# Kernel optimization log

Measured on AMD Instinct MI355X. Metric: run time of the kernel, lower is better.

Reference implementation:

```python
import jax, jax.numpy as jnp
import numpy as np

NUM_SRC = 200000
NUM_DST = 100000
NUM_EDGES = 1600000
IN_DIM = 128
HID = 256
OUT_DIM = 128


def layer_norm(h, g, b, eps=1e-5):
    mu = jnp.mean(h, axis=-1, keepdims=True)
    var = jnp.mean((h - mu) ** 2, axis=-1, keepdims=True)
    return (h - mu) * jax.lax.rsqrt(var + eps) * g + b


def setup_inputs() -> dict:
    key = jax.random.key(0)
    ks = jax.random.split(key, 8)
    s_in = 1.0 / np.sqrt(IN_DIM)
    s_hid = 1.0 / np.sqrt(HID)
    return {
        "x": jax.random.normal(ks[0], (NUM_SRC, IN_DIM), dtype=jnp.float32),
        "w_l": jax.random.normal(ks[1], (IN_DIM, HID), dtype=jnp.float32) * s_in,
        "b_l": jnp.zeros((HID,), dtype=jnp.float32),
        "w_r": jax.random.normal(ks[2], (IN_DIM, HID), dtype=jnp.float32) * s_in,
        "ln1_g": jnp.ones((HID,), dtype=jnp.float32),
        "ln1_b": jnp.zeros((HID,), dtype=jnp.float32),
        "w_out": jax.random.normal(ks[3], (HID, OUT_DIM), dtype=jnp.float32) * s_hid,
        "b_out": jnp.zeros((OUT_DIM,), dtype=jnp.float32),
        "ln2_g": jnp.ones((OUT_DIM,), dtype=jnp.float32),
        "ln2_b": jnp.zeros((OUT_DIM,), dtype=jnp.float32),
        "edge_src": jax.random.randint(ks[4], (NUM_EDGES,), 0, NUM_SRC, dtype=jnp.int64),
        "edge_dst": jax.random.randint(ks[5], (NUM_EDGES,), 0, NUM_DST, dtype=jnp.int64),
    }


def reference(x, w_l, b_l, w_r, ln1_g, ln1_b, w_out, b_out, ln2_g, ln2_b, edge_src, edge_dst):
    # SAGEConv bipartite: targets are the first NUM_DST rows of x
    x_tgt = x[:NUM_DST]
    # mean aggregation of source-node messages at destination nodes
    msgs = x[edge_src]  # [E, IN_DIM] irregular gather
    summed = jax.ops.segment_sum(msgs, edge_dst, num_segments=NUM_DST)
    cnt = jax.ops.segment_sum(jnp.ones((NUM_EDGES,), dtype=x.dtype), edge_dst, num_segments=NUM_DST)
    mean_nbr = summed / jnp.maximum(cnt, 1.0)[:, None]
    # out = lin_l(aggr) + lin_r(x_target); dropout p=0 is identity
    h = mean_nbr @ w_l + b_l + x_tgt @ w_r
    h = layer_norm(h, ln1_g, ln1_b)
    h = jax.nn.gelu(h, approximate=False)
    out = h @ w_out + b_out
    out = layer_norm(out, ln2_g, ln2_b)
    return out
```

## Files before the change

kernel.cpp:

```cpp
#include <hip/hip_runtime.h>
#include <math.h>

#define NSRC 200000
#define NDST 100000
#define NEDGE 1600000

typedef unsigned int uint32;
typedef unsigned short u16;

typedef short short8 __attribute__((ext_vector_type(8)));
typedef float f32x4 __attribute__((ext_vector_type(4)));

__device__ __forceinline__ u16 f2b(float f) {
  uint32 u = __float_as_uint(f);
  u += 0x7fffu + ((u >> 16) & 1u);
  return (u16)(u >> 16);
}
__device__ __forceinline__ float b2f_lo(uint32 u) { return __uint_as_float(u << 16); }
__device__ __forceinline__ float b2f_hi(uint32 u) { return __uint_as_float(u & 0xffff0000u); }

#define TM 32
#define NBKT 3125
#define BKTCAP 704
#define NB_H 64
#define EPH (NEDGE / NB_H)
#define NB_W 384
#define NB_CVT 25000

__global__ __launch_bounds__(256) void k_prep(const float* __restrict__ x, u16* __restrict__ xb,
                                              const float* __restrict__ wl,
                                              const float* __restrict__ wr,
                                              const float* __restrict__ wo,
                                              u16* __restrict__ wp1f, u16* __restrict__ wp2f,
                                              const int do_cvt, const int* __restrict__ src,
                                              const int* __restrict__ dst,
                                              int* __restrict__ bktcnt,
                                              int* __restrict__ pairs) {
  __shared__ int hist[NBKT];
  __shared__ int loff[NBKT];
  if (blockIdx.x < NB_H) {
    int base = blockIdx.x * EPH;
    for (int i = threadIdx.x; i < NBKT; i += 256) hist[i] = 0;
    __syncthreads();
    for (int i = threadIdx.x; i < EPH; i += 256) atomicAdd(&hist[dst[base + i] >> 5], 1);
    __syncthreads();
    {
      int start = (blockIdx.x * (NBKT / NB_H)) % NBKT;
      for (int j = threadIdx.x; j < NBKT; j += 256) {
        int i = j + start;
        if (i >= NBKT) i -= NBKT;
        int h = hist[i];
        loff[i] = h ? atomicAdd(&bktcnt[i * 16], h) : 0;
        hist[i] = 0;
      }
    }
    __syncthreads();
    for (int i = threadIdx.x; i < EPH; i += 256) {
      int d = dst[base + i];
      int s = src[base + i];
      int bin = d >> 5;
      int r = atomicAdd(&hist[bin], 1);
      int pos = loff[bin] + r;
      if (pos < BKTCAP) pairs[(size_t)bin * BKTCAP + pos] = (s << 5) | (d & 31);
    }
    return;
  }
  int bid = blockIdx.x - NB_H;
  if (bid < NB_W) {
    int t = bid * 256 + threadIdx.x;
    if (t < 65536) {
      int j = t & 7, lane = (t >> 3) & 63, nt = (t >> 9) & 3, kc = (t >> 11) & 7, w = t >> 14;
      int k = kc * 32 + (lane >> 4) * 8 + j;
      int n = w * 64 + nt * 16 + (lane & 15);
      float v = (k < 128) ? wl[k * 256 + n] : wr[(k - 128) * 256 + n];
      wp1f[t] = f2b(v);
    } else {
      int t2 = t - 65536;
      int j = t2 & 7, lane = (t2 >> 3) & 63, nt = (t2 >> 9) & 1, kc = (t2 >> 10) & 7, w = t2 >> 13;
      int k = kc * 32 + (lane >> 4) * 8 + j;
      int n = w * 32 + nt * 16 + (lane & 15);
      wp2f[t2] = f2b(wo[k * 128 + n]);
    }
    return;
  }
  if (!do_cvt) return;
  int idx = (bid - NB_W) * 256 + threadIdx.x;
  size_t i = (size_t)idx * 4;
  if (i < (size_t)NSRC * 128) {
    float4 f = *(const float4*)(x + i);
    uint2 o;
    o.x = (uint32)f2b(f.x) | ((uint32)f2b(f.y) << 16);
    o.y = (uint32)f2b(f.z) | ((uint32)f2b(f.w) << 16);
    *(uint2*)(xb + i) = o;
  }
}

#define LDAH 264
#define LCSR_LD 65

__global__ __launch_bounds__(512, 8) void k_fused(
    const u16* __restrict__ xb, const float* __restrict__ xf, const int x_is_bf16,
    const int* __restrict__ pairs, const int* __restrict__ bktcnt,
    const u16* __restrict__ wp1f, const u16* __restrict__ wp2f,
    const float* __restrict__ bl_g, const float* __restrict__ g1_g, const float* __restrict__ b1_g,
    const float* __restrict__ bo_g, const float* __restrict__ g2_g, const float* __restrict__ b2_g,
    float* __restrict__ out) {
  __shared__ __align__(16) u16 AH_lds[TM * LDAH];
  __shared__ float2 stats[8][16];
  __shared__ float2 stats2[TM];
  __shared__ int lcnt[TM];
  __shared__ int lcsr[TM * LCSR_LD];

  const int tid = threadIdx.x;
  const int wave = tid >> 6;
  const int lane = tid & 63;
  const int l15 = lane & 15;
  const int q = lane >> 4;
  const int wr = wave >> 2;
  const int wc = wave & 3;
  const int row0 = blockIdx.x * TM;

  {
    const int bkt = blockIdx.x;
    int total = bktcnt[(size_t)bkt * 16];
    int mp = total < BKTCAP ? total : BKTCAP;
    if (tid < TM) lcnt[tid] = 0;
    __syncthreads();
    for (int i = tid; i < mp; i += 512) {
      int v = pairs[(size_t)bkt * BKTCAP + i];
      int d5 = v & 31;
      int p = atomicAdd(&lcnt[d5], 1);
      if (p < 64) lcsr[d5 * LCSR_LD + p] = v >> 5;
    }
    __syncthreads();
  }

  {
    const int sub = tid & 15;
    const int r = tid >> 4;
    const int d = row0 + r;
    u16* rowp = AH_lds + r * LDAH;
    int n = lcnt[r];
    int m = n < 64 ? n : 64;
    const int* cp = lcsr + r * LCSR_LD;
    float a[8] = {0, 0, 0, 0, 0, 0, 0, 0};
    if (x_is_bf16) {
      int i = 0;
      for (; i + 3 < m; i += 4) {
        uint4 p[4];
#pragma unroll
        for (int u = 0; u < 4; u++)
          p[u] = *(const uint4*)(xb + (size_t)cp[i + u] * 128 + sub * 8);
#pragma unroll
        for (int u = 0; u < 4; u++) {
          a[0] += b2f_lo(p[u].x); a[1] += b2f_hi(p[u].x);
          a[2] += b2f_lo(p[u].y); a[3] += b2f_hi(p[u].y);
          a[4] += b2f_lo(p[u].z); a[5] += b2f_hi(p[u].z);
          a[6] += b2f_lo(p[u].w); a[7] += b2f_hi(p[u].w);
        }
      }
      for (; i < m; i++) {
        uint4 p = *(const uint4*)(xb + (size_t)cp[i] * 128 + sub * 8);
        a[0] += b2f_lo(p.x); a[1] += b2f_hi(p.x);
        a[2] += b2f_lo(p.y); a[3] += b2f_hi(p.y);
        a[4] += b2f_lo(p.z); a[5] += b2f_hi(p.z);
        a[6] += b2f_lo(p.w); a[7] += b2f_hi(p.w);
      }
    } else {
      for (int i = 0; i < m; i++) {
        int s = cp[i];
        const float* p = xf + (size_t)s * 128 + sub * 8;
        float4 f0 = *(const float4*)p;
        float4 f1 = *(const float4*)(p + 4);
        a[0] += f0.x; a[1] += f0.y; a[2] += f0.z; a[3] += f0.w;
        a[4] += f1.x; a[5] += f1.y; a[6] += f1.z; a[7] += f1.w;
      }
    }
    float sc = 1.f / (float)(n > 0 ? n : 1);
    uint4 o;
    o.x = (uint32)f2b(a[0] * sc) | ((uint32)f2b(a[1] * sc) << 16);
    o.y = (uint32)f2b(a[2] * sc) | ((uint32)f2b(a[3] * sc) << 16);
    o.z = (uint32)f2b(a[4] * sc) | ((uint32)f2b(a[5] * sc) << 16);
    o.w = (uint32)f2b(a[6] * sc) | ((uint32)f2b(a[7] * sc) << 16);
    *(uint4*)(rowp + sub * 8) = o;
    uint4 xv;
    if (x_is_bf16) {
      xv = *(const uint4*)(xb + (size_t)d * 128 + sub * 8);
    } else {
      const float* p = xf + (size_t)d * 128 + sub * 8;
      float4 f0 = *(const float4*)p;
      float4 f1 = *(const float4*)(p + 4);
      xv.x = (uint32)f2b(f0.x) | ((uint32)f2b(f0.y) << 16);
      xv.y = (uint32)f2b(f0.z) | ((uint32)f2b(f0.w) << 16);
      xv.z = (uint32)f2b(f1.x) | ((uint32)f2b(f1.y) << 16);
      xv.w = (uint32)f2b(f1.z) | ((uint32)f2b(f1.w) << 16);
    }
    *(uint4*)(rowp + 128 + sub * 8) = xv;
  }
  __syncthreads();

  f32x4 acc[4];
#pragma unroll
  for (int j = 0; j < 4; j++) acc[j] = (f32x4){0.f, 0.f, 0.f, 0.f};

#pragma unroll 1
  for (int kc = 0; kc < 8; kc++) {
    short8 bfr[4];
    const uint4* bsrc = (const uint4*)(wp1f + (((size_t)wc * 8 + kc) * 4) * 512);
#pragma unroll
    for (int nt = 0; nt < 4; nt++) bfr[nt] = ((const short8*)(bsrc + nt * 64))[lane];
    short8 af = *(const short8*)(AH_lds + (16 * wr + l15) * LDAH + kc * 32 + q * 8);
#pragma unroll
    for (int nt = 0; nt < 4; nt++)
      acc[nt] = __builtin_amdgcn_mfma_f32_16x16x32_bf16(af, bfr[nt], acc[nt], 0, 0, 0);
  }

  float bl[4], g1[4], b1[4];
#pragma unroll
  for (int nt = 0; nt < 4; nt++) {
    int c = 64 * wc + 16 * nt + l15;
    bl[nt] = bl_g[c]; g1[nt] = g1_g[c]; b1[nt] = b1_g[c];
  }
#pragma unroll
  for (int nt = 0; nt < 4; nt++)
#pragma unroll
    for (int r = 0; r < 4; r++) acc[nt][r] += bl[nt];

#pragma unroll
  for (int r = 0; r < 4; r++) {
    float s = 0.f, s2 = 0.f;
#pragma unroll
    for (int nt = 0; nt < 4; nt++) { float v = acc[nt][r]; s += v; s2 += v * v; }
#pragma unroll
    for (int m = 1; m < 16; m <<= 1) { s += __shfl_xor(s, m, 64); s2 += __shfl_xor(s2, m, 64); }
    if (l15 == 0) stats[wave][4 * q + r] = make_float2(s, s2);
  }
  __syncthreads();
  if (tid < TM) {
    int wr_ = tid >> 4, rl = tid & 15;
    float S = 0.f, Q = 0.f;
#pragma unroll
    for (int w = 0; w < 4; w++) { float2 t = stats[wr_ * 4 + w][rl]; S += t.x; Q += t.y; }
    float mu = S * (1.f / 256.f);
    float var = Q * (1.f / 256.f) - mu * mu;
    stats2[tid] = make_float2(mu, rsqrtf(var + 1e-5f));
  }
  __syncthreads();
#pragma unroll
  for (int r = 0; r < 4; r++) {
    int row = 16 * wr + 4 * q + r;
    float2 st = stats2[row];
#pragma unroll
    for (int nt = 0; nt < 4; nt++) {
      float v = acc[nt][r];
      float hn = (v - st.x) * st.y * g1[nt] + b1[nt];
      float t2 = hn * hn;
      float u = fmaf(0.044715f * t2, hn, hn);
      float ge = hn / (1.f + __expf(-1.5957691216f * u));
      AH_lds[row * LDAH + 64 * wc + 16 * nt + l15] = f2b(ge);
    }
  }
  __syncthreads();

  f32x4 acc2[2];
#pragma unroll
  for (int j = 0; j < 2; j++) acc2[j] = (f32x4){0.f, 0.f, 0.f, 0.f};

#pragma unroll 1
  for (int kc = 0; kc < 8; kc++) {
    short8 bfr[2];
    const uint4* bsrc = (const uint4*)(wp2f + (((size_t)wc * 8 + kc) * 2) * 512);
#pragma unroll
    for (int nt = 0; nt < 2; nt++) bfr[nt] = ((const short8*)(bsrc + nt * 64))[lane];
    short8 af = *(const short8*)(AH_lds + (16 * wr + l15) * LDAH + kc * 32 + q * 8);
#pragma unroll
    for (int nt = 0; nt < 2; nt++)
      acc2[nt] = __builtin_amdgcn_mfma_f32_16x16x32_bf16(af, bfr[nt], acc2[nt], 0, 0, 0);
  }

  float bo[2], g2[2], b2c[2];
#pragma unroll
  for (int nt = 0; nt < 2; nt++) {
    int c = 32 * wc + 16 * nt + l15;
    bo[nt] = bo_g[c]; g2[nt] = g2_g[c]; b2c[nt] = b2_g[c];
  }
#pragma unroll
  for (int nt = 0; nt < 2; nt++)
#pragma unroll
    for (int r = 0; r < 4; r++) acc2[nt][r] += bo[nt];

#pragma unroll
  for (int r = 0; r < 4; r++) {
    float s = 0.f, s2 = 0.f;
#pragma unroll
    for (int nt = 0; nt < 2; nt++) { float v = acc2[nt][r]; s += v; s2 += v * v; }
#pragma unroll
    for (int m = 1; m < 16; m <<= 1) { s += __shfl_xor(s, m, 64); s2 += __shfl_xor(s2, m, 64); }
    if (l15 == 0) stats[wave][4 * q + r] = make_float2(s, s2);
  }
  __syncthreads();
  if (tid < TM) {
    int wr_ = tid >> 4, rl = tid & 15;
    float S = 0.f, Q = 0.f;
#pragma unroll
    for (int w = 0; w < 4; w++) { float2 t = stats[wr_ * 4 + w][rl]; S += t.x; Q += t.y; }
    float mu = S * (1.f / 128.f);
    float var = Q * (1.f / 128.f) - mu * mu;
    stats2[tid] = make_float2(mu, rsqrtf(var + 1e-5f));
  }
  __syncthreads();
#pragma unroll
  for (int r = 0; r < 4; r++) {
    int row = 16 * wr + 4 * q + r;
    float2 st = stats2[row];
#pragma unroll
    for (int nt = 0; nt < 2; nt++) {
      float v = acc2[nt][r];
      out[(size_t)(row0 + row) * 128 + 32 * wc + 16 * nt + l15] =
          (v - st.x) * st.y * g2[nt] + b2c[nt];
    }
  }
}

extern "C" void kernel_launch(void* const* d_in, const int* in_sizes, int n_in,
                              void* d_out, int out_size, void* d_ws, size_t ws_size,
                              hipStream_t stream) {
  const float* x   = (const float*)d_in[0];
  const float* w_l = (const float*)d_in[1];
  const float* b_l = (const float*)d_in[2];
  const float* w_r = (const float*)d_in[3];
  const float* g1  = (const float*)d_in[4];
  const float* b1  = (const float*)d_in[5];
  const float* w_o = (const float*)d_in[6];
  const float* b_o = (const float*)d_in[7];
  const float* g2  = (const float*)d_in[8];
  const float* b2  = (const float*)d_in[9];
  const int* esrc  = (const int*)d_in[10];
  const int* edst  = (const int*)d_in[11];
  float* out = (float*)d_out;

  char* ws = (char*)d_ws;
  size_t off = 0;
  auto alloc = [&](size_t bytes) -> void* {
    off = (off + 255) & ~(size_t)255;
    void* p = ws + off;
    off += bytes;
    return p;
  };
  int* bktcnt = (int*)alloc((size_t)NBKT * 16 * 4);
  u16* wp1f   = (u16*)alloc((size_t)65536 * 2);
  u16* wp2f   = (u16*)alloc((size_t)32768 * 2);
  int* pairs  = (int*)alloc((size_t)NBKT * BKTCAP * 4);

  size_t rem = (ws_size > off + 512) ? (ws_size - off - 512) : 0;
  size_t xb_bytes = (size_t)NSRC * 128 * 2;
  int x_is_bf16 = (rem >= xb_bytes) ? 1 : 0;
  u16* xb = x_is_bf16 ? (u16*)alloc(xb_bytes) : nullptr;

  hipMemsetAsync(bktcnt, 0, (size_t)NBKT * 16 * 4, stream);
  k_prep<<<NB_H + NB_W + NB_CVT, 256, 0, stream>>>(x, xb, w_l, w_r, w_o, wp1f, wp2f,
                                                   x_is_bf16, esrc, edst, bktcnt, pairs);
  k_fused<<<NBKT, 512, 0, stream>>>(xb, x, x_is_bf16, pairs, bktcnt, wp1f, wp2f,
                                    b_l, g1, b1, b_o, g2, b2, out);
}
```

Before: 409.0 us.

## Double fused-kernel row tile to 64 rows with 1024-thread blocks and 64-wide buckets

Each fused block now handles 64 destination rows with 1024 threads instead of 32 rows with 512, and the edge bucketing in the prep kernel switches to 64-row buckets with larger capacity and more histogram blocks. The aim is to amortize each block's weight-fragment loads and bucket setup over more rows, and to parallelize the histogram pass across more blocks. Bounds guards handle the partial last tile. In exchange, blocks use more LDS and registers, which can lower occupancy. The staggered start that spread bucket-counter atomics across blocks is removed, and the larger bucket capacity could still overflow in rare cases.

```diff
diff --git a/kernel.cpp b/kernel.cpp
--- a/kernel.cpp
+++ b/kernel.cpp
@@ -19,10 +19,9 @@
 __device__ __forceinline__ float b2f_lo(uint32 u) { return __uint_as_float(u << 16); }
 __device__ __forceinline__ float b2f_hi(uint32 u) { return __uint_as_float(u & 0xffff0000u); }
 
-#define TM 32
-#define NBKT 3125
-#define BKTCAP 704
-#define NB_H 64
+#define NBKT 1563
+#define BKTCAP 1344
+#define NB_H 256
 #define EPH (NEDGE / NB_H)
 #define NB_W 384
 #define NB_CVT 25000
@@ -42,26 +41,21 @@
     int base = blockIdx.x * EPH;
     for (int i = threadIdx.x; i < NBKT; i += 256) hist[i] = 0;
     __syncthreads();
-    for (int i = threadIdx.x; i < EPH; i += 256) atomicAdd(&hist[dst[base + i] >> 5], 1);
-    __syncthreads();
-    {
-      int start = (blockIdx.x * (NBKT / NB_H)) % NBKT;
-      for (int j = threadIdx.x; j < NBKT; j += 256) {
-        int i = j + start;
-        if (i >= NBKT) i -= NBKT;
-        int h = hist[i];
-        loff[i] = h ? atomicAdd(&bktcnt[i * 16], h) : 0;
-        hist[i] = 0;
-      }
+    for (int i = threadIdx.x; i < EPH; i += 256) atomicAdd(&hist[dst[base + i] >> 6], 1);
+    __syncthreads();
+    for (int i = threadIdx.x; i < NBKT; i += 256) {
+      int h = hist[i];
+      loff[i] = h ? atomicAdd(&bktcnt[i * 16], h) : 0;
+      hist[i] = 0;
     }
     __syncthreads();
     for (int i = threadIdx.x; i < EPH; i += 256) {
       int d = dst[base + i];
       int s = src[base + i];
-      int bin = d >> 5;
+      int bin = d >> 6;
       int r = atomicAdd(&hist[bin], 1);
       int pos = loff[bin] + r;
-      if (pos < BKTCAP) pairs[(size_t)bin * BKTCAP + pos] = (s << 5) | (d & 31);
+      if (pos < BKTCAP) pairs[(size_t)bin * BKTCAP + pos] = (s << 6) | (d & 63);
     }
     return;
   }
@@ -98,18 +92,18 @@
 #define LDAH 264
 #define LCSR_LD 65
 
-__global__ __launch_bounds__(512, 8) void k_fused(
+__global__ __launch_bounds__(1024, 8) void k_fused(
     const u16* __restrict__ xb, const float* __restrict__ xf, const int x_is_bf16,
     const int* __restrict__ pairs, const int* __restrict__ bktcnt,
     const u16* __restrict__ wp1f, const u16* __restrict__ wp2f,
     const float* __restrict__ bl_g, const float* __restrict__ g1_g, const float* __restrict__ b1_g,
     const float* __restrict__ bo_g, const float* __restrict__ g2_g, const float* __restrict__ b2_g,
     float* __restrict__ out) {
-  __shared__ __align__(16) u16 AH_lds[TM * LDAH];
-  __shared__ float2 stats[8][16];
-  __shared__ float2 stats2[TM];
-  __shared__ int lcnt[TM];
-  __shared__ int lcsr[TM * LCSR_LD];
+  __shared__ __align__(16) u16 AH_lds[64 * LDAH];
+  __shared__ float2 stats[16][16];
+  __shared__ float2 stats2[64];
+  __shared__ int lcnt[64];
+  __shared__ int lcsr[64 * LCSR_LD];
 
   const int tid = threadIdx.x;
   const int wave = tid >> 6;
@@ -118,19 +112,19 @@
   const int q = lane >> 4;
   const int wr = wave >> 2;
   const int wc = wave & 3;
-  const int row0 = blockIdx.x * TM;
+  const int row0 = blockIdx.x * 64;
 
   {
     const int bkt = blockIdx.x;
     int total = bktcnt[(size_t)bkt * 16];
     int mp = total < BKTCAP ? total : BKTCAP;
-    if (tid < TM) lcnt[tid] = 0;
-    __syncthreads();
-    for (int i = tid; i < mp; i += 512) {
+    if (tid < 64) lcnt[tid] = 0;
+    __syncthreads();
+    for (int i = tid; i < mp; i += 1024) {
       int v = pairs[(size_t)bkt * BKTCAP + i];
-      int d5 = v & 31;
-      int p = atomicAdd(&lcnt[d5], 1);
-      if (p < 64) lcsr[d5 * LCSR_LD + p] = v >> 5;
+      int d6 = v & 63;
+      int p = atomicAdd(&lcnt[d6], 1);
+      if (p < 64) lcsr[d6 * LCSR_LD + p] = v >> 6;
     }
     __syncthreads();
   }
@@ -140,62 +134,68 @@
     const int r = tid >> 4;
     const int d = row0 + r;
     u16* rowp = AH_lds + r * LDAH;
-    int n = lcnt[r];
-    int m = n < 64 ? n : 64;
-    const int* cp = lcsr + r * LCSR_LD;
-    float a[8] = {0, 0, 0, 0, 0, 0, 0, 0};
-    if (x_is_bf16) {
-      int i = 0;
-      for (; i + 3 < m; i += 4) {
-        uint4 p[4];
-#pragma unroll
-        for (int u = 0; u < 4; u++)
-          p[u] = *(const uint4*)(xb + (size_t)cp[i + u] * 128 + sub * 8);
-#pragma unroll
-        for (int u = 0; u < 4; u++) {
-          a[0] += b2f_lo(p[u].x); a[1] += b2f_hi(p[u].x);
-          a[2] += b2f_lo(p[u].y); a[3] += b2f_hi(p[u].y);
-          a[4] += b2f_lo(p[u].z); a[5] += b2f_hi(p[u].z);
-          a[6] += b2f_lo(p[u].w); a[7] += b2f_hi(p[u].w);
+    if (d < NDST) {
+      int n = lcnt[r];
+      int m = n < 64 ? n : 64;
+      const int* cp = lcsr + r * LCSR_LD;
+      float a[8] = {0, 0, 0, 0, 0, 0, 0, 0};
+      if (x_is_bf16) {
+        int i = 0;
+        for (; i + 3 < m; i += 4) {
+          uint4 p[4];
+#pragma unroll
+          for (int u = 0; u < 4; u++)
+            p[u] = *(const uint4*)(xb + (size_t)cp[i + u] * 128 + sub * 8);
+#pragma unroll
+          for (int u = 0; u < 4; u++) {
+            a[0] += b2f_lo(p[u].x); a[1] += b2f_hi(p[u].x);
+            a[2] += b2f_lo(p[u].y); a[3] += b2f_hi(p[u].y);
+            a[4] += b2f_lo(p[u].z); a[5] += b2f_hi(p[u].z);
+            a[6] += b2f_lo(p[u].w); a[7] += b2f_hi(p[u].w);
+          }
+        }
+        for (; i < m; i++) {
+          uint4 p = *(const uint4*)(xb + (size_t)cp[i] * 128 + sub * 8);
+          a[0] += b2f_lo(p.x); a[1] += b2f_hi(p.x);
+          a[2] += b2f_lo(p.y); a[3] += b2f_hi(p.y);
+          a[4] += b2f_lo(p.z); a[5] += b2f_hi(p.z);
+          a[6] += b2f_lo(p.w); a[7] += b2f_hi(p.w);
+        }
+      } else {
+        for (int i = 0; i < m; i++) {
+          int s = cp[i];
+          const float* p = xf + (size_t)s * 128 + sub * 8;
+          float4 f0 = *(const float4*)p;
+          float4 f1 = *(const float4*)(p + 4);
+          a[0] += f0.x; a[1] += f0.y; a[2] += f0.z; a[3] += f0.w;
+          a[4] += f1.x; a[5] += f1.y; a[6] += f1.z; a[7] += f1.w;
         }
       }
-      for (; i < m; i++) {
-        uint4 p = *(const uint4*)(xb + (size_t)cp[i] * 128 + sub * 8);
-        a[0] += b2f_lo(p.x); a[1] += b2f_hi(p.x);
-        a[2] += b2f_lo(p.y); a[3] += b2f_hi(p.y);
-        a[4] += b2f_lo(p.z); a[5] += b2f_hi(p.z);
-        a[6] += b2f_lo(p.w); a[7] += b2f_hi(p.w);
-      }
-    } else {
-      for (int i = 0; i < m; i++) {
-        int s = cp[i];
-        const float* p = xf + (size_t)s * 128 + sub * 8;
+      float sc = 1.f / (float)(n > 0 ? n : 1);
+      uint4 o;
+      o.x = (uint32)f2b(a[0] * sc) | ((uint32)f2b(a[1] * sc) << 16);
+      o.y = (uint32)f2b(a[2] * sc) | ((uint32)f2b(a[3] * sc) << 16);
+      o.z = (uint32)f2b(a[4] * sc) | ((uint32)f2b(a[5] * sc) << 16);
+      o.w = (uint32)f2b(a[6] * sc) | ((uint32)f2b(a[7] * sc) << 16);
+      *(uint4*)(rowp + sub * 8) = o;
+      uint4 xv;
+      if (x_is_bf16) {
+        xv = *(const uint4*)(xb + (size_t)d * 128 + sub * 8);
+      } else {
+        const float* p = xf + (size_t)d * 128 + sub * 8;
         float4 f0 = *(const float4*)p;
         float4 f1 = *(const float4*)(p + 4);
-        a[0] += f0.x; a[1] += f0.y; a[2] += f0.z; a[3] += f0.w;
-        a[4] += f1.x; a[5] += f1.y; a[6] += f1.z; a[7] += f1.w;
+        xv.x = (uint32)f2b(f0.x) | ((uint32)f2b(f0.y) << 16);
+        xv.y = (uint32)f2b(f0.z) | ((uint32)f2b(f0.w) << 16);
+        xv.z = (uint32)f2b(f1.x) | ((uint32)f2b(f1.y) << 16);
+        xv.w = (uint32)f2b(f1.z) | ((uint32)f2b(f1.w) << 16);
       }
-    }
-    float sc = 1.f / (float)(n > 0 ? n : 1);
-    uint4 o;
-    o.x = (uint32)f2b(a[0] * sc) | ((uint32)f2b(a[1] * sc) << 16);
-    o.y = (uint32)f2b(a[2] * sc) | ((uint32)f2b(a[3] * sc) << 16);
-    o.z = (uint32)f2b(a[4] * sc) | ((uint32)f2b(a[5] * sc) << 16);
-    o.w = (uint32)f2b(a[6] * sc) | ((uint32)f2b(a[7] * sc) << 16);
-    *(uint4*)(rowp + sub * 8) = o;
-    uint4 xv;
-    if (x_is_bf16) {
-      xv = *(const uint4*)(xb + (size_t)d * 128 + sub * 8);
+      *(uint4*)(rowp + 128 + sub * 8) = xv;
     } else {
-      const float* p = xf + (size_t)d * 128 + sub * 8;
-      float4 f0 = *(const float4*)p;
-      float4 f1 = *(const float4*)(p + 4);
-      xv.x = (uint32)f2b(f0.x) | ((uint32)f2b(f0.y) << 16);
-      xv.y = (uint32)f2b(f0.z) | ((uint32)f2b(f0.w) << 16);
-      xv.z = (uint32)f2b(f1.x) | ((uint32)f2b(f1.y) << 16);
-      xv.w = (uint32)f2b(f1.z) | ((uint32)f2b(f1.w) << 16);
-    }
-    *(uint4*)(rowp + 128 + sub * 8) = xv;
+      uint4 z = {0u, 0u, 0u, 0u};
+      *(uint4*)(rowp + sub * 8) = z;
+      *(uint4*)(rowp + 128 + sub * 8) = z;
+    }
   }
   __syncthreads();
 
@@ -236,7 +236,7 @@
     if (l15 == 0) stats[wave][4 * q + r] = make_float2(s, s2);
   }
   __syncthreads();
-  if (tid < TM) {
+  if (tid < 64) {
     int wr_ = tid >> 4, rl = tid & 15;
     float S = 0.f, Q = 0.f;
 #pragma unroll
@@ -299,7 +299,7 @@
     if (l15 == 0) stats[wave][4 * q + r] = make_float2(s, s2);
   }
   __syncthreads();
-  if (tid < TM) {
+  if (tid < 64) {
     int wr_ = tid >> 4, rl = tid & 15;
     float S = 0.f, Q = 0.f;
 #pragma unroll
@@ -312,12 +312,14 @@
 #pragma unroll
   for (int r = 0; r < 4; r++) {
     int row = 16 * wr + 4 * q + r;
-    float2 st = stats2[row];
-#pragma unroll
-    for (int nt = 0; nt < 2; nt++) {
-      float v = acc2[nt][r];
-      out[(size_t)(row0 + row) * 128 + 32 * wc + 16 * nt + l15] =
-          (v - st.x) * st.y * g2[nt] + b2c[nt];
+    int R = row0 + row;
+    if (R < NDST) {
+      float2 st = stats2[row];
+#pragma unroll
+      for (int nt = 0; nt < 2; nt++) {
+        float v = acc2[nt][r];
+        out[(size_t)R * 128 + 32 * wc + 16 * nt + l15] = (v - st.x) * st.y * g2[nt] + b2c[nt];
+      }
     }
   }
 }
@@ -360,6 +362,6 @@
   hipMemsetAsync(bktcnt, 0, (size_t)NBKT * 16 * 4, stream);
   k_prep<<<NB_H + NB_W + NB_CVT, 256, 0, stream>>>(x, xb, w_l, w_r, w_o, wp1f, wp2f,
                                                    x_is_bf16, esrc, edst, bktcnt, pairs);
-  k_fused<<<NBKT, 512, 0, stream>>>(xb, x, x_is_bf16, pairs, bktcnt, wp1f, wp2f,
-                                    b_l, g1, b1, b_o, g2, b2, out);
+  k_fused<<<NBKT, 1024, 0, stream>>>(xb, x, x_is_bf16, pairs, bktcnt, wp1f, wp2f,
+                                     b_l, g1, b1, b_o, g2, b2, out);
 }
```

After: 348.2 us. 1.17x faster.
